# Kernel tuning notes

Measured on AMD Instinct MI355X. Metric: run time of the kernel, lower is better.

The kernel has to match this reference:

```python
import jax, jax.numpy as jnp
import numpy as np

N = 50000      # nodes
E = 800000     # edges (before self-loops)
DIN = 128      # in_channels
DH = 64        # hidden_channels
HEADS = 2
DOUT = 64      # out_channels
NEG_SLOPE = 0.2  # PyG GATConv leaky_relu slope


def setup_inputs() -> dict:
    key = jax.random.key(0)
    ks = jax.random.split(key, 10)
    node_emb = jax.random.normal(ks[0], (N, DIN), dtype=jnp.float32)
    edge_index = jax.random.randint(ks[1], (2, E), 0, N, dtype=jnp.int64)
    # conv1: in -> hidden, heads=2, concat=True
    W1 = jax.random.normal(ks[2], (DIN, HEADS * DH), dtype=jnp.float32) / np.sqrt(DIN)
    att_src1 = jax.random.normal(ks[3], (HEADS, DH), dtype=jnp.float32) * 0.1
    att_dst1 = jax.random.normal(ks[4], (HEADS, DH), dtype=jnp.float32) * 0.1
    b1 = jnp.zeros((HEADS * DH,), dtype=jnp.float32)
    # conv2: hidden*heads -> out, heads=1, concat=False
    W2 = jax.random.normal(ks[5], (HEADS * DH, 1 * DOUT), dtype=jnp.float32) / np.sqrt(HEADS * DH)
    att_src2 = jax.random.normal(ks[6], (1, DOUT), dtype=jnp.float32) * 0.1
    att_dst2 = jax.random.normal(ks[7], (1, DOUT), dtype=jnp.float32) * 0.1
    b2 = jnp.zeros((DOUT,), dtype=jnp.float32)
    return {"node_emb": node_emb, "edge_index": edge_index,
            "W1": W1, "att_src1": att_src1, "att_dst1": att_dst1, "b1": b1,
            "W2": W2, "att_src2": att_src2, "att_dst2": att_dst2, "b2": b2}


def gat_layer(x, src, dst, W, att_src, att_dst, bias, heads, concat, n):
    # x: [N, Fin]; W: [Fin, heads*C]; att_*: [heads, C]
    C = W.shape[1] // heads
    h = (x @ W).reshape(n, heads, C)                       # [N, H, C]
    a_src = jnp.einsum('nhc,hc->nh', h, att_src)           # [N, H]
    a_dst = jnp.einsum('nhc,hc->nh', h, att_dst)           # [N, H]
    e = jax.nn.leaky_relu(a_src[src] + a_dst[dst], NEG_SLOPE)  # [E, H]
    # segment softmax over incoming edges of each destination node
    m = jax.ops.segment_max(e, dst, num_segments=n)        # [N, H]
    ex = jnp.exp(e - m[dst])
    denom = jax.ops.segment_sum(ex, dst, num_segments=n)   # [N, H]
    alpha = ex / denom[dst]                                # [E, H]
    out = jax.ops.segment_sum(h[src] * alpha[:, :, None], dst, num_segments=n)  # [N, H, C]
    if concat:
        out = out.reshape(n, heads * C)
    else:
        out = out.mean(axis=1)
    return out + bias


def reference(node_emb, edge_index, W1, att_src1, att_dst1, b1, W2, att_src2, att_dst2, b2):
    loops = jnp.arange(N, dtype=edge_index.dtype)
    src = jnp.concatenate([edge_index[0], loops])  # PyG add_self_loops=True
    dst = jnp.concatenate([edge_index[1], loops])
    h = gat_layer(node_emb, src, dst, W1, att_src1, att_dst1, b1, HEADS, True, N)
    h = jax.nn.elu(h)
    # dropout is identity in eval mode
    out = gat_layer(h, src, dst, W2, att_src2, att_dst2, b2, 1, False, N)
    return out
```

## Files before the change

### kernel.cpp

```cpp
#include <hip/hip_runtime.h>
#include <hip/hip_fp16.h>
#include <math.h>

constexpr float NEG_SLOPE = 0.2f;
constexpr int NPART = 8;
constexpr int WSLOT = 16;

__device__ inline __half2 u2h(unsigned int u) { return *reinterpret_cast<__half2*>(&u); }
__device__ inline unsigned int h2u(__half2 h) { return *reinterpret_cast<unsigned int*>(&h); }

__device__ inline void fmamix8(uint4 v, float al, float* acc) {
    float2 f0 = __half22float2(u2h(v.x)), f1 = __half22float2(u2h(v.y));
    float2 f2 = __half22float2(u2h(v.z)), f3 = __half22float2(u2h(v.w));
    acc[0] = fmaf(al, f0.x, acc[0]); acc[1] = fmaf(al, f0.y, acc[1]);
    acc[2] = fmaf(al, f1.x, acc[2]); acc[3] = fmaf(al, f1.y, acc[3]);
    acc[4] = fmaf(al, f2.x, acc[4]); acc[5] = fmaf(al, f2.y, acc[5]);
    acc[6] = fmaf(al, f3.x, acc[6]); acc[7] = fmaf(al, f3.y, acc[7]);
}

__device__ inline int ell_resolve(const unsigned short* __restrict__ ell,
                                  const int* pre, int node, int n, int l) {
    int p = 0;
#pragma unroll
    for (int t = 1; t < NPART; t++)
        if (l >= pre[t]) p = t;
    int slot = l - pre[p];
    return (int)ell[((size_t)p * n + node) * WSLOT + slot];
}

__global__ __launch_bounds__(256) void k_fused1(
    const int* __restrict__ src, const int* __restrict__ dst, int e, int S, int G,
    int* __restrict__ cur, unsigned short* __restrict__ ell,
    const float* __restrict__ x, const float* __restrict__ W,
    const float* __restrict__ a_src, const float* __restrict__ a_dst,
    __half* __restrict__ h1h, float* __restrict__ att, int n) {
    __shared__ float xs[32 * 128];
    __shared__ __half wsh[128 * 128];
    int bid = blockIdx.x;
    int t = threadIdx.x;

    int third = bid / 3;
    bool interleave = (2 * S <= G + 2);
    bool isScat = interleave ? ((bid % 3 == 0) && (third < S)) : (bid < S);
    if (isScat) {
        int sid = interleave ? third : bid;
        int p = bid & (NPART - 1);
        int i0 = (sid * 256 + t) * 4;
        if (i0 + 3 < e) {
            int4 d4 = *reinterpret_cast<const int4*>(dst + i0);
            int4 s4 = *reinterpret_cast<const int4*>(src + i0);
            int a0 = atomicAdd(&cur[p * n + d4.x], 1);
            int a1 = atomicAdd(&cur[p * n + d4.y], 1);
            int a2 = atomicAdd(&cur[p * n + d4.z], 1);
            int a3 = atomicAdd(&cur[p * n + d4.w], 1);
            if (a0 < WSLOT) ell[((size_t)p * n + d4.x) * WSLOT + a0] = (unsigned short)s4.x;
            if (a1 < WSLOT) ell[((size_t)p * n + d4.y) * WSLOT + a1] = (unsigned short)s4.y;
            if (a2 < WSLOT) ell[((size_t)p * n + d4.z) * WSLOT + a2] = (unsigned short)s4.z;
            if (a3 < WSLOT) ell[((size_t)p * n + d4.w) * WSLOT + a3] = (unsigned short)s4.w;
        } else {
            for (int i = i0; i < e; i++) {
                int d = dst[i];
                int slot = atomicAdd(&cur[p * n + d], 1);
                if (slot < WSLOT) ell[((size_t)p * n + d) * WSLOT + slot] = (unsigned short)src[i];
            }
        }
        return;
    }
    int gid = interleave ? (bid - min(S, (bid + 2) / 3)) : (bid - S);
    if (gid >= G) return;

    const float4* Wv = (const float4*)W;
    uint2* wsv = (uint2*)wsh;
#pragma unroll
    for (int i = 0; i < 16; i++) {
        float4 w = Wv[t + 256 * i];
        __half2 a = __floats2half2_rn(w.x, w.y);
        __half2 b = __floats2half2_rn(w.z, w.w);
        uint2 o; o.x = h2u(a); o.y = h2u(b);
        wsv[t + 256 * i] = o;
    }
    int row0 = gid * 32;
    const float4* xv = (const float4*)x;
    float4* xsv = (float4*)xs;
#pragma unroll
    for (int ii = 0; ii < 4; ii++) {
        int i = t + 256 * ii;
        int r = i >> 5, c4 = i & 31;
        int gr = row0 + r;
        float4 v = (gr < n) ? xv[(size_t)gr * 32 + c4] : make_float4(0.f, 0.f, 0.f, 0.f);
        xsv[i] = v;
    }
    __syncthreads();
    int tc = t & 31;
    int tr = t >> 5;
    float acc[4][4];
#pragma unroll
    for (int i = 0; i < 4; i++)
#pragma unroll
        for (int j = 0; j < 4; j++) acc[i][j] = 0.f;
    const uint2* wsv2 = (const uint2*)wsh;
    for (int k = 0; k < 128; k++) {
        uint2 wu = wsv2[k * 32 + tc];
        float2 wA = __half22float2(u2h(wu.x));
        float2 wB = __half22float2(u2h(wu.y));
#pragma unroll
        for (int i = 0; i < 4; i++) {
            float xvv = xs[(tr * 4 + i) * 128 + k];
            acc[i][0] = fmaf(xvv, wA.x, acc[i][0]);
            acc[i][1] = fmaf(xvv, wA.y, acc[i][1]);
            acc[i][2] = fmaf(xvv, wB.x, acc[i][2]);
            acc[i][3] = fmaf(xvv, wB.y, acc[i][3]);
        }
    }
#pragma unroll
    for (int i = 0; i < 4; i++) {
        int gr = row0 + tr * 4 + i;
        if (gr < n) {
            __half2 p01 = __floats2half2_rn(acc[i][0], acc[i][1]);
            __half2 p23 = __floats2half2_rn(acc[i][2], acc[i][3]);
            uint2 o; o.x = h2u(p01); o.y = h2u(p23);
            *reinterpret_cast<uint2*>(h1h + (size_t)gr * 128 + 4 * tc) = o;
        }
    }
    const float4* asv = (const float4*)a_src;
    const float4* adv = (const float4*)a_dst;
    float4 as4 = asv[tc], ad4 = adv[tc];
    int lane = t & 63;
#pragma unroll
    for (int i = 0; i < 4; i++) {
        float s = acc[i][0] * as4.x + acc[i][1] * as4.y + acc[i][2] * as4.z + acc[i][3] * as4.w;
        float d = acc[i][0] * ad4.x + acc[i][1] * ad4.y + acc[i][2] * ad4.z + acc[i][3] * ad4.w;
#pragma unroll
        for (int o = 1; o < 16; o <<= 1) {
            s += __shfl_xor(s, o);
            d += __shfl_xor(d, o);
        }
        float s1 = __shfl(s, (lane & 32) + 16);
        float d1 = __shfl(d, (lane & 32) + 16);
        int gr = row0 + tr * 4 + i;
        if ((lane & 31) == 0 && gr < n) {
            ((float4*)att)[gr] = make_float4(s, s1, d, d1);
        }
    }
}

__global__ __launch_bounds__(256) void k_gemm2(const __half* __restrict__ x2h,
                                               const float* __restrict__ W,
                                               const float* __restrict__ a_src,
                                               const float* __restrict__ a_dst,
                                               __half* __restrict__ h2h,
                                               float* __restrict__ att, int n) {
    __shared__ float xs[32 * 128];
    __shared__ __half wsh[128 * 64];
    int t = threadIdx.x;
    const float4* Wv = (const float4*)W;
    uint2* wsv = (uint2*)wsh;
#pragma unroll
    for (int i = 0; i < 8; i++) {
        float4 w = Wv[t + 256 * i];
        __half2 a = __floats2half2_rn(w.x, w.y);
        __half2 b = __floats2half2_rn(w.z, w.w);
        uint2 o; o.x = h2u(a); o.y = h2u(b);
        wsv[t + 256 * i] = o;
    }
    int row0 = blockIdx.x * 32;
    const uint2* xv = (const uint2*)x2h;
    float4* xsv = (float4*)xs;
#pragma unroll
    for (int ii = 0; ii < 4; ii++) {
        int i = t + 256 * ii;
        int r = i >> 5, c4 = i & 31;
        int gr = row0 + r;
        uint2 u = (gr < n) ? xv[(size_t)gr * 32 + c4] : make_uint2(0u, 0u);
        float2 lo = __half22float2(u2h(u.x)), hi = __half22float2(u2h(u.y));
        xsv[i] = make_float4(lo.x, lo.y, hi.x, hi.y);
    }
    __syncthreads();
    int tc = t & 15;
    int tr = t >> 4;
    float acc[2][4];
#pragma unroll
    for (int i = 0; i < 2; i++)
#pragma unroll
        for (int j = 0; j < 4; j++) acc[i][j] = 0.f;
    const uint2* wsv2 = (const uint2*)wsh;
    for (int k = 0; k < 128; k++) {
        uint2 wu = wsv2[k * 16 + tc];
        float2 wA = __half22float2(u2h(wu.x));
        float2 wB = __half22float2(u2h(wu.y));
#pragma unroll
        for (int i = 0; i < 2; i++) {
            float xvv = xs[(tr * 2 + i) * 128 + k];
            acc[i][0] = fmaf(xvv, wA.x, acc[i][0]);
            acc[i][1] = fmaf(xvv, wA.y, acc[i][1]);
            acc[i][2] = fmaf(xvv, wB.x, acc[i][2]);
            acc[i][3] = fmaf(xvv, wB.y, acc[i][3]);
        }
    }
#pragma unroll
    for (int i = 0; i < 2; i++) {
        int gr = row0 + tr * 2 + i;
        if (gr < n) {
            __half2 p01 = __floats2half2_rn(acc[i][0], acc[i][1]);
            __half2 p23 = __floats2half2_rn(acc[i][2], acc[i][3]);
            uint2 o; o.x = h2u(p01); o.y = h2u(p23);
            *reinterpret_cast<uint2*>(h2h + (size_t)gr * 64 + 4 * tc) = o;
        }
    }
    const float4* asv = (const float4*)a_src;
    const float4* adv = (const float4*)a_dst;
    float4 as4 = asv[tc], ad4 = adv[tc];
#pragma unroll
    for (int i = 0; i < 2; i++) {
        float s = acc[i][0] * as4.x + acc[i][1] * as4.y + acc[i][2] * as4.z + acc[i][3] * as4.w;
        float d = acc[i][0] * ad4.x + acc[i][1] * ad4.y + acc[i][2] * ad4.z + acc[i][3] * ad4.w;
#pragma unroll
        for (int o = 1; o < 16; o <<= 1) {
            s += __shfl_xor(s, o);
            d += __shfl_xor(d, o);
        }
        int gr = row0 + tr * 2 + i;
        if (tc == 0 && gr < n) {
            ((float2*)att)[gr] = make_float2(s, d);
        }
    }
}

__global__ __launch_bounds__(256) void k_aggr1(const int* __restrict__ cur,
                                               const unsigned short* __restrict__ ell,
                                               const float* __restrict__ att,
                                               const __half* __restrict__ h1h,
                                               const float* __restrict__ bias,
                                               __half* __restrict__ x2h, int n) {
    int wid = threadIdx.x >> 6, lane = threadIdx.x & 63;
    int node = blockIdx.x * 4 + wid;
    if (node >= n) return;

    int cnt = 0;
    if (lane < NPART) cnt = cur[lane * n + node];
    int pre[NPART];
    int tot = 1;
#pragma unroll
    for (int p = 0; p < NPART; p++) {
        int cc = __shfl(cnt, p);
        cc = cc < WSLOT ? cc : WSLOT;
        pre[p] = tot;
        tot += cc;
    }

    const float4* attv = (const float4*)att;
    float4 an = attv[node];
    float ad0 = an.z, ad1 = an.w;

    int chq = lane & 15;
    int g = lane >> 4;
    bool hsel = (chq >= 8);

    float f[8];

    if (tot <= 64) {
        int c = node;
        float p0 = 0.f, p1 = 0.f;
        if (lane < tot) {
            if (lane > 0) c = ell_resolve(ell, pre, node, n, lane);
            float4 a = attv[c];
            float e0 = a.x + ad0; e0 = e0 > 0.f ? e0 : NEG_SLOPE * e0;
            float e1 = a.y + ad1; e1 = e1 > 0.f ? e1 : NEG_SLOPE * e1;
            p0 = __expf(e0); p1 = __expf(e1);
        }
        float sum0 = p0, sum1 = p1;
#pragma unroll
        for (int d = 1; d < 64; d <<= 1) {
            sum0 += __shfl_xor(sum0, d);
            sum1 += __shfl_xor(sum1, d);
        }
        float rsel = hsel ? (1.f / sum1) : (1.f / sum0);

        __half2 z = __float2half2_rn(0.f);
        __half2 hacc0 = z, hacc1 = z, hacc2 = z, hacc3 = z;
        for (int k0 = 0; k0 < tot; k0 += 16) {
            uint4 v[4];
            __half2 al2[4];
#pragma unroll
            for (int u = 0; u < 4; u++) {
                int k = k0 + 4 * u + g;
                int ks = k & 63;
                int sn = __shfl(c, ks);
                float pa = __shfl(p0, ks);
                float pb = __shfl(p1, ks);
                float alf = (k < tot) ? (hsel ? pb : pa) * rsel : 0.f;
                al2[u] = __float2half2_rn(alf);
                v[u] = *reinterpret_cast<const uint4*>(h1h + (size_t)sn * 128 + 8 * chq);
            }
#pragma unroll
            for (int u = 0; u < 4; u++) {
                hacc0 = __hfma2(al2[u], u2h(v[u].x), hacc0);
                hacc1 = __hfma2(al2[u], u2h(v[u].y), hacc1);
                hacc2 = __hfma2(al2[u], u2h(v[u].z), hacc2);
                hacc3 = __hfma2(al2[u], u2h(v[u].w), hacc3);
            }
        }
        f[0] = __low2float(hacc0); f[1] = __high2float(hacc0);
        f[2] = __low2float(hacc1); f[3] = __high2float(hacc1);
        f[4] = __low2float(hacc2); f[5] = __high2float(hacc2);
        f[6] = __low2float(hacc3); f[7] = __high2float(hacc3);
    } else {
        float sum0 = 0.f, sum1 = 0.f;
        for (int l = lane; l < tot; l += 64) {
            int c = (l == 0) ? node : ell_resolve(ell, pre, node, n, l);
            float4 a = attv[c];
            float e0 = a.x + ad0; e0 = e0 > 0.f ? e0 : NEG_SLOPE * e0;
            float e1 = a.y + ad1; e1 = e1 > 0.f ? e1 : NEG_SLOPE * e1;
            sum0 += __expf(e0); sum1 += __expf(e1);
        }
#pragma unroll
        for (int d = 1; d < 64; d <<= 1) {
            sum0 += __shfl_xor(sum0, d);
            sum1 += __shfl_xor(sum1, d);
        }
        float rsel = hsel ? (1.f / sum1) : (1.f / sum0);
        float acc[8];
#pragma unroll
        for (int i = 0; i < 8; i++) acc[i] = 0.f;
        for (int j = 0; j < tot; j += 4) {
            int l = j + g;
            bool valid = (l < tot);
            int lc = valid ? l : 0;
            int sn = (lc == 0) ? node : ell_resolve(ell, pre, node, n, lc);
            float4 a = attv[sn];
            float e0 = a.x + ad0; e0 = e0 > 0.f ? e0 : NEG_SLOPE * e0;
            float e1 = a.y + ad1; e1 = e1 > 0.f ? e1 : NEG_SLOPE * e1;
            float pp = hsel ? __expf(e1) : __expf(e0);
            float al = valid ? pp * rsel : 0.f;
            uint4 v = *reinterpret_cast<const uint4*>(h1h + (size_t)sn * 128 + 8 * chq);
            fmamix8(v, al, acc);
        }
#pragma unroll
        for (int i = 0; i < 8; i++) f[i] = acc[i];
    }

#pragma unroll
    for (int i = 0; i < 8; i++) {
        f[i] += __shfl_xor(f[i], 16);
        f[i] += __shfl_xor(f[i], 32);
    }
    if (lane < 16) {
        const float4* bv = (const float4*)bias;
        float4 bA = bv[2 * chq], bB = bv[2 * chq + 1];
        float o[8];
        o[0] = f[0] + bA.x; o[1] = f[1] + bA.y;
        o[2] = f[2] + bA.z; o[3] = f[3] + bA.w;
        o[4] = f[4] + bB.x; o[5] = f[5] + bB.y;
        o[6] = f[6] + bB.z; o[7] = f[7] + bB.w;
#pragma unroll
        for (int i = 0; i < 8; i++) o[i] = o[i] > 0.f ? o[i] : (__expf(o[i]) - 1.f);
        __half2 q01 = __floats2half2_rn(o[0], o[1]);
        __half2 q23 = __floats2half2_rn(o[2], o[3]);
        __half2 q45 = __floats2half2_rn(o[4], o[5]);
        __half2 q67 = __floats2half2_rn(o[6], o[7]);
        uint4 w; w.x = h2u(q01); w.y = h2u(q23); w.z = h2u(q45); w.w = h2u(q67);
        *reinterpret_cast<uint4*>(x2h + (size_t)node * 128 + 8 * chq) = w;
    }
}

__global__ __launch_bounds__(256) void k_aggr2(const int* __restrict__ cur,
                                               const unsigned short* __restrict__ ell,
                                               const float* __restrict__ att,
                                               const __half* __restrict__ h2h,
                                               const float* __restrict__ bias,
                                               float* __restrict__ out, int n) {
    int wid = threadIdx.x >> 6, lane = threadIdx.x & 63;
    int node = blockIdx.x * 4 + wid;
    if (node >= n) return;

    int cnt = 0;
    if (lane < NPART) cnt = cur[lane * n + node];
    int pre[NPART];
    int tot = 1;
#pragma unroll
    for (int p = 0; p < NPART; p++) {
        int cc = __shfl(cnt, p);
        cc = cc < WSLOT ? cc : WSLOT;
        pre[p] = tot;
        tot += cc;
    }

    const float2* attv = (const float2*)att;
    float adn = attv[node].y;
    int chq = lane & 7;
    int g = lane >> 3;

    float f[8];

    if (tot <= 64) {
        int c = node;
        float p = 0.f;
        if (lane < tot) {
            if (lane > 0) c = ell_resolve(ell, pre, node, n, lane);
            float e = attv[c].x + adn;
            e = e > 0.f ? e : NEG_SLOPE * e;
            p = __expf(e);
        }
        float sum = p;
#pragma unroll
        for (int d = 1; d < 64; d <<= 1) sum += __shfl_xor(sum, d);
        float r = 1.f / sum;

        __half2 z = __float2half2_rn(0.f);
        __half2 hacc0 = z, hacc1 = z, hacc2 = z, hacc3 = z;
        for (int k0 = 0; k0 < tot; k0 += 16) {
            uint4 v[2];
            __half2 al2[2];
#pragma unroll
            for (int u = 0; u < 2; u++) {
                int k = k0 + 8 * u + g;
                int ks = k & 63;
                int sn = __shfl(c, ks);
                float pk = __shfl(p, ks);
                float alf = (k < tot) ? pk * r : 0.f;
                al2[u] = __float2half2_rn(alf);
                v[u] = *reinterpret_cast<const uint4*>(h2h + (size_t)sn * 64 + 8 * chq);
            }
#pragma unroll
            for (int u = 0; u < 2; u++) {
                hacc0 = __hfma2(al2[u], u2h(v[u].x), hacc0);
                hacc1 = __hfma2(al2[u], u2h(v[u].y), hacc1);
                hacc2 = __hfma2(al2[u], u2h(v[u].z), hacc2);
                hacc3 = __hfma2(al2[u], u2h(v[u].w), hacc3);
            }
        }
        f[0] = __low2float(hacc0); f[1] = __high2float(hacc0);
        f[2] = __low2float(hacc1); f[3] = __high2float(hacc1);
        f[4] = __low2float(hacc2); f[5] = __high2float(hacc2);
        f[6] = __low2float(hacc3); f[7] = __high2float(hacc3);
    } else {
        float sum = 0.f;
        for (int l = lane; l < tot; l += 64) {
            int c = (l == 0) ? node : ell_resolve(ell, pre, node, n, l);
            float e = attv[c].x + adn;
            e = e > 0.f ? e : NEG_SLOPE * e;
            sum += __expf(e);
        }
#pragma unroll
        for (int d = 1; d < 64; d <<= 1) sum += __shfl_xor(sum, d);
        float r = 1.f / sum;
        float acc[8];
#pragma unroll
        for (int i = 0; i < 8; i++) acc[i] = 0.f;
        for (int j = 0; j < tot; j += 8) {
            int l = j + g;
            bool valid = (l < tot);
            int lc = valid ? l : 0;
            int sn = (lc == 0) ? node : ell_resolve(ell, pre, node, n, lc);
            float e = attv[sn].x + adn;
            e = e > 0.f ? e : NEG_SLOPE * e;
            float al = valid ? __expf(e) * r : 0.f;
            uint4 v = *reinterpret_cast<const uint4*>(h2h + (size_t)sn * 64 + 8 * chq);
            fmamix8(v, al, acc);
        }
#pragma unroll
        for (int i = 0; i < 8; i++) f[i] = acc[i];
    }

#pragma unroll
    for (int i = 0; i < 8; i++) {
        f[i] += __shfl_xor(f[i], 8);
        f[i] += __shfl_xor(f[i], 16);
        f[i] += __shfl_xor(f[i], 32);
    }
    if (lane < 8) {
        const float4* bv = (const float4*)bias;
        float4 bA = bv[2 * chq], bB = bv[2 * chq + 1];
        float4* ov = (float4*)(out + (size_t)node * 64 + 8 * chq);
        ov[0] = make_float4(f[0] + bA.x, f[1] + bA.y, f[2] + bA.z, f[3] + bA.w);
        ov[1] = make_float4(f[4] + bB.x, f[5] + bB.y, f[6] + bB.z, f[7] + bB.w);
    }
}

extern "C" void kernel_launch(void* const* d_in, const int* in_sizes, int n_in,
                              void* d_out, int out_size, void* d_ws, size_t ws_size,
                              hipStream_t stream) {
    const float* x    = (const float*)d_in[0];
    const int*   ei   = (const int*)d_in[1];
    const float* W1   = (const float*)d_in[2];
    const float* asr1 = (const float*)d_in[3];
    const float* adt1 = (const float*)d_in[4];
    const float* b1   = (const float*)d_in[5];
    const float* W2   = (const float*)d_in[6];
    const float* asr2 = (const float*)d_in[7];
    const float* adt2 = (const float*)d_in[8];
    const float* b2   = (const float*)d_in[9];
    float* out = (float*)d_out;

    const int N = in_sizes[0] / 128;
    const int E = in_sizes[1] / 2;
    const int* srcI = ei;
    const int* dstI = ei + E;

    char* p = (char*)d_ws;
    auto alloc = [&](size_t b) -> void* {
        void* r = (void*)p;
        p += ((b + 255) / 256) * 256;
        return r;
    };
    int* cur = (int*)alloc(sizeof(int) * (size_t)NPART * N);
    unsigned short* ell = (unsigned short*)alloc(sizeof(unsigned short) *
                                                 (size_t)NPART * N * WSLOT);
    __half* h1h = (__half*)alloc(sizeof(__half) * (size_t)N * 128);
    float* att1 = (float*)alloc(sizeof(float) * (size_t)N * 4);
    __half* x2h = (__half*)alloc(sizeof(__half) * (size_t)N * 128);
    __half* h2h = (__half*)alloc(sizeof(__half) * (size_t)N * 64);
    float* att2 = (float*)alloc(sizeof(float) * (size_t)N * 2);

    int S = (E + 1023) / 1024;
    int G = (N + 31) / 32;
    int nbNode4 = (N + 3) / 4;
    int nbRow32 = (N + 31) / 32;

    hipMemsetAsync(cur, 0, sizeof(int) * (size_t)NPART * N, stream);

    k_fused1<<<S + G, 256, 0, stream>>>(srcI, dstI, E, S, G, cur, ell,
                                        x, W1, asr1, adt1, h1h, att1, N);

    k_aggr1<<<nbNode4, 256, 0, stream>>>(cur, ell, att1, h1h, b1, x2h, N);

    k_gemm2<<<nbRow32, 256, 0, stream>>>(x2h, W2, asr2, adt2, h2h, att2, N);
    k_aggr2<<<nbNode4, 256, 0, stream>>>(cur, ell, att2, h2h, b2, out, N);
}
```

Measured before the change: 146.3 us.

## Use fp16 dot2 GEMMs with pre-transposed weights and XCC-based scatter partitions

Adds a small kernel that converts W1/W2 to fp16 transposed layout once per call. Both GEMMs then keep fp16 x and W tiles in shared memory and use the fdot2 instruction on 8-element vectors, which removes per-block weight conversion and halves shared-memory traffic. The column mapping changes to strided columns, so h1h/h2h are now written as scalar half stores. The edge scatter picks its partition from the hardware XCC id instead of the block id, keeping atomics local to one die's L2. The risks are fp16 products feeding fp32 accumulation, an extra launch, and less coalesced output stores.

```diff
diff --git a/kernel.cpp b/kernel.cpp
--- a/kernel.cpp
+++ b/kernel.cpp
@@ -6,8 +6,30 @@
 constexpr int NPART = 8;
 constexpr int WSLOT = 16;
 
+typedef _Float16 __attribute__((ext_vector_type(2))) h2v;
+
 __device__ inline __half2 u2h(unsigned int u) { return *reinterpret_cast<__half2*>(&u); }
 __device__ inline unsigned int h2u(__half2 h) { return *reinterpret_cast<unsigned int*>(&h); }
+
+__device__ inline float dot8(uint4 a, uint4 b, float c) {
+#if __has_builtin(__builtin_amdgcn_fdot2)
+    c = __builtin_amdgcn_fdot2(__builtin_bit_cast(h2v, a.x), __builtin_bit_cast(h2v, b.x), c, false);
+    c = __builtin_amdgcn_fdot2(__builtin_bit_cast(h2v, a.y), __builtin_bit_cast(h2v, b.y), c, false);
+    c = __builtin_amdgcn_fdot2(__builtin_bit_cast(h2v, a.z), __builtin_bit_cast(h2v, b.z), c, false);
+    c = __builtin_amdgcn_fdot2(__builtin_bit_cast(h2v, a.w), __builtin_bit_cast(h2v, b.w), c, false);
+#else
+    float2 fa, fb;
+    fa = __half22float2(u2h(a.x)); fb = __half22float2(u2h(b.x));
+    c = fmaf(fa.x, fb.x, c); c = fmaf(fa.y, fb.y, c);
+    fa = __half22float2(u2h(a.y)); fb = __half22float2(u2h(b.y));
+    c = fmaf(fa.x, fb.x, c); c = fmaf(fa.y, fb.y, c);
+    fa = __half22float2(u2h(a.z)); fb = __half22float2(u2h(b.z));
+    c = fmaf(fa.x, fb.x, c); c = fmaf(fa.y, fb.y, c);
+    fa = __half22float2(u2h(a.w)); fb = __half22float2(u2h(b.w));
+    c = fmaf(fa.x, fb.x, c); c = fmaf(fa.y, fb.y, c);
+#endif
+    return c;
+}
 
 __device__ inline void fmamix8(uint4 v, float al, float* acc) {
     float2 f0 = __half22float2(u2h(v.x)), f1 = __half22float2(u2h(v.y));
@@ -28,14 +50,29 @@
     return (int)ell[((size_t)p * n + node) * WSLOT + slot];
 }
 
+__global__ void k_wt(const float* __restrict__ W1, const float* __restrict__ W2,
+                     __half* __restrict__ Wt1, __half* __restrict__ Wt2) {
+    int id = blockIdx.x * 256 + threadIdx.x;
+    if (id < 128 * 128) {
+        int col = id >> 7, k = id & 127;
+        Wt1[id] = __float2half(W1[k * 128 + col]);
+    } else {
+        int j = id - 128 * 128;
+        if (j < 64 * 128) {
+            int col = j >> 7, k = j & 127;
+            Wt2[j] = __float2half(W2[k * 64 + col]);
+        }
+    }
+}
+
 __global__ __launch_bounds__(256) void k_fused1(
     const int* __restrict__ src, const int* __restrict__ dst, int e, int S, int G,
     int* __restrict__ cur, unsigned short* __restrict__ ell,
-    const float* __restrict__ x, const float* __restrict__ W,
+    const float* __restrict__ x, const __half* __restrict__ Wt1,
     const float* __restrict__ a_src, const float* __restrict__ a_dst,
     __half* __restrict__ h1h, float* __restrict__ att, int n) {
-    __shared__ float xs[32 * 128];
-    __shared__ __half wsh[128 * 128];
+    __shared__ __half xsh[32 * 128];
+    __shared__ __half wsh[128 * 72];
     int bid = blockIdx.x;
     int t = threadIdx.x;
 
@@ -44,7 +81,9 @@
     bool isScat = interleave ? ((bid % 3 == 0) && (third < S)) : (bid < S);
     if (isScat) {
         int sid = interleave ? third : bid;
-        int p = bid & (NPART - 1);
+        unsigned xcc;
+        asm volatile("s_getreg_b32 %0, hwreg(HW_REG_XCC_ID)" : "=s"(xcc));
+        int p = (int)(xcc & (NPART - 1));
         int i0 = (sid * 256 + t) * 4;
         if (i0 + 3 < e) {
             int4 d4 = *reinterpret_cast<const int4*>(dst + i0);
@@ -69,157 +108,156 @@
     int gid = interleave ? (bid - min(S, (bid + 2) / 3)) : (bid - S);
     if (gid >= G) return;
 
-    const float4* Wv = (const float4*)W;
-    uint2* wsv = (uint2*)wsh;
-#pragma unroll
-    for (int i = 0; i < 16; i++) {
-        float4 w = Wv[t + 256 * i];
-        __half2 a = __floats2half2_rn(w.x, w.y);
-        __half2 b = __floats2half2_rn(w.z, w.w);
-        uint2 o; o.x = h2u(a); o.y = h2u(b);
-        wsv[t + 256 * i] = o;
-    }
     int row0 = gid * 32;
+    int tc = t & 31;
+    int tr = t >> 5;
+
     const float4* xv = (const float4*)x;
-    float4* xsv = (float4*)xs;
 #pragma unroll
     for (int ii = 0; ii < 4; ii++) {
         int i = t + 256 * ii;
         int r = i >> 5, c4 = i & 31;
         int gr = row0 + r;
         float4 v = (gr < n) ? xv[(size_t)gr * 32 + c4] : make_float4(0.f, 0.f, 0.f, 0.f);
-        xsv[i] = v;
-    }
-    __syncthreads();
-    int tc = t & 31;
-    int tr = t >> 5;
+        __half2 a = __floats2half2_rn(v.x, v.y);
+        __half2 b = __floats2half2_rn(v.z, v.w);
+        uint2 o; o.x = h2u(a); o.y = h2u(b);
+        *reinterpret_cast<uint2*>(xsh + r * 128 + c4 * 4) = o;
+    }
+
     float acc[4][4];
 #pragma unroll
     for (int i = 0; i < 4; i++)
 #pragma unroll
         for (int j = 0; j < 4; j++) acc[i][j] = 0.f;
-    const uint2* wsv2 = (const uint2*)wsh;
-    for (int k = 0; k < 128; k++) {
-        uint2 wu = wsv2[k * 32 + tc];
-        float2 wA = __half22float2(u2h(wu.x));
-        float2 wB = __half22float2(u2h(wu.y));
-#pragma unroll
-        for (int i = 0; i < 4; i++) {
-            float xvv = xs[(tr * 4 + i) * 128 + k];
-            acc[i][0] = fmaf(xvv, wA.x, acc[i][0]);
-            acc[i][1] = fmaf(xvv, wA.y, acc[i][1]);
-            acc[i][2] = fmaf(xvv, wB.x, acc[i][2]);
-            acc[i][3] = fmaf(xvv, wB.y, acc[i][3]);
-        }
-    }
+
+#pragma unroll
+    for (int kh = 0; kh < 2; kh++) {
+        __syncthreads();
+#pragma unroll
+        for (int ii = 0; ii < 4; ii++) {
+            int i = t + 256 * ii;
+            int col = i >> 3, kg = i & 7;
+            uint4 w = *reinterpret_cast<const uint4*>(Wt1 + col * 128 + kh * 64 + kg * 8);
+            *reinterpret_cast<uint4*>(wsh + col * 72 + kg * 8) = w;
+        }
+        __syncthreads();
+#pragma unroll
+        for (int k8 = 0; k8 < 8; k8++) {
+            int kbase = kh * 64 + k8 * 8;
+            uint4 ax[4], wx[4];
+#pragma unroll
+            for (int i = 0; i < 4; i++)
+                ax[i] = *reinterpret_cast<const uint4*>(xsh + (4 * tr + i) * 128 + kbase);
+#pragma unroll
+            for (int j = 0; j < 4; j++)
+                wx[j] = *reinterpret_cast<const uint4*>(wsh + (tc + 32 * j) * 72 + k8 * 8);
+#pragma unroll
+            for (int i = 0; i < 4; i++)
+#pragma unroll
+                for (int j = 0; j < 4; j++)
+                    acc[i][j] = dot8(ax[i], wx[j], acc[i][j]);
+        }
+    }
+
+    float as0 = a_src[tc], as1 = a_src[tc + 32], as2 = a_src[tc + 64], as3 = a_src[tc + 96];
+    float ad0 = a_dst[tc], ad1 = a_dst[tc + 32], ad2 = a_dst[tc + 64], ad3 = a_dst[tc + 96];
 #pragma unroll
     for (int i = 0; i < 4; i++) {
-        int gr = row0 + tr * 4 + i;
+        int gr = row0 + 4 * tr + i;
         if (gr < n) {
-            __half2 p01 = __floats2half2_rn(acc[i][0], acc[i][1]);
-            __half2 p23 = __floats2half2_rn(acc[i][2], acc[i][3]);
-            uint2 o; o.x = h2u(p01); o.y = h2u(p23);
-            *reinterpret_cast<uint2*>(h1h + (size_t)gr * 128 + 4 * tc) = o;
-        }
-    }
-    const float4* asv = (const float4*)a_src;
-    const float4* adv = (const float4*)a_dst;
-    float4 as4 = asv[tc], ad4 = adv[tc];
-    int lane = t & 63;
-#pragma unroll
-    for (int i = 0; i < 4; i++) {
-        float s = acc[i][0] * as4.x + acc[i][1] * as4.y + acc[i][2] * as4.z + acc[i][3] * as4.w;
-        float d = acc[i][0] * ad4.x + acc[i][1] * ad4.y + acc[i][2] * ad4.z + acc[i][3] * ad4.w;
-#pragma unroll
-        for (int o = 1; o < 16; o <<= 1) {
-            s += __shfl_xor(s, o);
-            d += __shfl_xor(d, o);
-        }
-        float s1 = __shfl(s, (lane & 32) + 16);
-        float d1 = __shfl(d, (lane & 32) + 16);
-        int gr = row0 + tr * 4 + i;
-        if ((lane & 31) == 0 && gr < n) {
-            ((float4*)att)[gr] = make_float4(s, s1, d, d1);
+#pragma unroll
+            for (int j = 0; j < 4; j++)
+                h1h[(size_t)gr * 128 + tc + 32 * j] = __float2half(acc[i][j]);
+        }
+        float s0 = acc[i][0] * as0 + acc[i][1] * as1;
+        float s1 = acc[i][2] * as2 + acc[i][3] * as3;
+        float d0 = acc[i][0] * ad0 + acc[i][1] * ad1;
+        float d1 = acc[i][2] * ad2 + acc[i][3] * ad3;
+#pragma unroll
+        for (int o = 1; o < 32; o <<= 1) {
+            s0 += __shfl_xor(s0, o);
+            s1 += __shfl_xor(s1, o);
+            d0 += __shfl_xor(d0, o);
+            d1 += __shfl_xor(d1, o);
+        }
+        if (tc == 0 && gr < n) {
+            ((float4*)att)[gr] = make_float4(s0, s1, d0, d1);
         }
     }
 }
 
 __global__ __launch_bounds__(256) void k_gemm2(const __half* __restrict__ x2h,
-                                               const float* __restrict__ W,
+                                               const __half* __restrict__ Wt2,
                                                const float* __restrict__ a_src,
                                                const float* __restrict__ a_dst,
                                                __half* __restrict__ h2h,
                                                float* __restrict__ att, int n) {
-    __shared__ float xs[32 * 128];
-    __shared__ __half wsh[128 * 64];
+    __shared__ __half xsh[32 * 128];
+    __shared__ __half wsh[64 * 136];
     int t = threadIdx.x;
-    const float4* Wv = (const float4*)W;
-    uint2* wsv = (uint2*)wsh;
-#pragma unroll
-    for (int i = 0; i < 8; i++) {
-        float4 w = Wv[t + 256 * i];
-        __half2 a = __floats2half2_rn(w.x, w.y);
-        __half2 b = __floats2half2_rn(w.z, w.w);
-        uint2 o; o.x = h2u(a); o.y = h2u(b);
-        wsv[t + 256 * i] = o;
-    }
     int row0 = blockIdx.x * 32;
-    const uint2* xv = (const uint2*)x2h;
-    float4* xsv = (float4*)xs;
+    int tc = t & 15;
+    int tr = t >> 4;
+
+#pragma unroll
+    for (int ii = 0; ii < 2; ii++) {
+        int i = t + 256 * ii;
+        int r = i >> 4, g8 = i & 15;
+        int gr = row0 + r;
+        uint4 v = (gr < n) ? *reinterpret_cast<const uint4*>(x2h + (size_t)gr * 128 + g8 * 8)
+                           : make_uint4(0u, 0u, 0u, 0u);
+        *reinterpret_cast<uint4*>(xsh + r * 128 + g8 * 8) = v;
+    }
 #pragma unroll
     for (int ii = 0; ii < 4; ii++) {
         int i = t + 256 * ii;
-        int r = i >> 5, c4 = i & 31;
-        int gr = row0 + r;
-        uint2 u = (gr < n) ? xv[(size_t)gr * 32 + c4] : make_uint2(0u, 0u);
-        float2 lo = __half22float2(u2h(u.x)), hi = __half22float2(u2h(u.y));
-        xsv[i] = make_float4(lo.x, lo.y, hi.x, hi.y);
+        int col = i >> 4, kg = i & 15;
+        uint4 w = *reinterpret_cast<const uint4*>(Wt2 + col * 128 + kg * 8);
+        *reinterpret_cast<uint4*>(wsh + col * 136 + kg * 8) = w;
     }
     __syncthreads();
-    int tc = t & 15;
-    int tr = t >> 4;
+
     float acc[2][4];
 #pragma unroll
     for (int i = 0; i < 2; i++)
 #pragma unroll
         for (int j = 0; j < 4; j++) acc[i][j] = 0.f;
-    const uint2* wsv2 = (const uint2*)wsh;
-    for (int k = 0; k < 128; k++) {
-        uint2 wu = wsv2[k * 16 + tc];
-        float2 wA = __half22float2(u2h(wu.x));
-        float2 wB = __half22float2(u2h(wu.y));
-#pragma unroll
-        for (int i = 0; i < 2; i++) {
-            float xvv = xs[(tr * 2 + i) * 128 + k];
-            acc[i][0] = fmaf(xvv, wA.x, acc[i][0]);
-            acc[i][1] = fmaf(xvv, wA.y, acc[i][1]);
-            acc[i][2] = fmaf(xvv, wB.x, acc[i][2]);
-            acc[i][3] = fmaf(xvv, wB.y, acc[i][3]);
-        }
-    }
+
+#pragma unroll
+    for (int k8 = 0; k8 < 16; k8++) {
+        uint4 ax[2], wx[4];
+#pragma unroll
+        for (int i = 0; i < 2; i++)
+            ax[i] = *reinterpret_cast<const uint4*>(xsh + (2 * tr + i) * 128 + k8 * 8);
+#pragma unroll
+        for (int j = 0; j < 4; j++)
+            wx[j] = *reinterpret_cast<const uint4*>(wsh + (tc + 16 * j) * 136 + k8 * 8);
+#pragma unroll
+        for (int i = 0; i < 2; i++)
+#pragma unroll
+            for (int j = 0; j < 4; j++)
+                acc[i][j] = dot8(ax[i], wx[j], acc[i][j]);
+    }
+
+    float as[4], ad[4];
+#pragma unroll
+    for (int j = 0; j < 4; j++) { as[j] = a_src[tc + 16 * j]; ad[j] = a_dst[tc + 16 * j]; }
 #pragma unroll
     for (int i = 0; i < 2; i++) {
-        int gr = row0 + tr * 2 + i;
+        int gr = row0 + 2 * tr + i;
         if (gr < n) {
-            __half2 p01 = __floats2half2_rn(acc[i][0], acc[i][1]);
-            __half2 p23 = __floats2half2_rn(acc[i][2], acc[i][3]);
-            uint2 o; o.x = h2u(p01); o.y = h2u(p23);
-            *reinterpret_cast<uint2*>(h2h + (size_t)gr * 64 + 4 * tc) = o;
-        }
-    }
-    const float4* asv = (const float4*)a_src;
-    const float4* adv = (const float4*)a_dst;
-    float4 as4 = asv[tc], ad4 = adv[tc];
-#pragma unroll
-    for (int i = 0; i < 2; i++) {
-        float s = acc[i][0] * as4.x + acc[i][1] * as4.y + acc[i][2] * as4.z + acc[i][3] * as4.w;
-        float d = acc[i][0] * ad4.x + acc[i][1] * ad4.y + acc[i][2] * ad4.z + acc[i][3] * ad4.w;
+#pragma unroll
+            for (int j = 0; j < 4; j++)
+                h2h[(size_t)gr * 64 + tc + 16 * j] = __float2half(acc[i][j]);
+        }
+        float s = acc[i][0] * as[0] + acc[i][1] * as[1] + acc[i][2] * as[2] + acc[i][3] * as[3];
+        float d = acc[i][0] * ad[0] + acc[i][1] * ad[1] + acc[i][2] * ad[2] + acc[i][3] * ad[3];
 #pragma unroll
         for (int o = 1; o < 16; o <<= 1) {
             s += __shfl_xor(s, o);
             d += __shfl_xor(d, o);
         }
-        int gr = row0 + tr * 2 + i;
         if (tc == 0 && gr < n) {
             ((float2*)att)[gr] = make_float2(s, d);
         }
@@ -511,6 +549,8 @@
     __half* x2h = (__half*)alloc(sizeof(__half) * (size_t)N * 128);
     __half* h2h = (__half*)alloc(sizeof(__half) * (size_t)N * 64);
     float* att2 = (float*)alloc(sizeof(float) * (size_t)N * 2);
+    __half* Wt1 = (__half*)alloc(sizeof(__half) * 128 * 128);
+    __half* Wt2 = (__half*)alloc(sizeof(__half) * 64 * 128);
 
     int S = (E + 1023) / 1024;
     int G = (N + 31) / 32;
@@ -519,11 +559,13 @@
 
     hipMemsetAsync(cur, 0, sizeof(int) * (size_t)NPART * N, stream);
 
+    k_wt<<<96, 256, 0, stream>>>(W1, W2, Wt1, Wt2);
+
     k_fused1<<<S + G, 256, 0, stream>>>(srcI, dstI, E, S, G, cur, ell,
-                                        x, W1, asr1, adt1, h1h, att1, N);
+                                        x, Wt1, asr1, adt1, h1h, att1, N);
 
     k_aggr1<<<nbNode4, 256, 0, stream>>>(cur, ell, att1, h1h, b1, x2h, N);
 
-    k_gemm2<<<nbRow32, 256, 0, stream>>>(x2h, W2, asr2, adt2, h2h, att2, N);
+    k_gemm2<<<nbRow32, 256, 0, stream>>>(x2h, Wt2, asr2, adt2, h2h, att2, N);
     k_aggr2<<<nbNode4, 256, 0, stream>>>(cur, ell, att2, h2h, b2, out, N);
 }
```

Result: slower. 161.0 us (+10.1%).

## Interleave ELL partitions per node and stage W in two halves

Applied to the files above, without the earlier changes.

Changes the per-partition count and ELL neighbor arrays from partition-major to node-major. All partitions of a destination node now sit next to each other, so the aggregation kernels read counts and neighbor slots from one contiguous region instead of eight strided ones. Separately, the GEMM block now converts and stages the weight matrix in two 64-row halves with extra barriers, halving its shared memory to raise occupancy. The cost is an extra sync round and a reload of shared memory per half. Scatter atomics from different partitions may now contend on nearby cache lines.

```diff
diff --git a/kernel.cpp b/kernel.cpp
--- a/kernel.cpp
+++ b/kernel.cpp
@@ -19,13 +19,13 @@
 }
 
 __device__ inline int ell_resolve(const unsigned short* __restrict__ ell,
-                                  const int* pre, int node, int n, int l) {
+                                  const int* pre, int node, int l) {
     int p = 0;
 #pragma unroll
     for (int t = 1; t < NPART; t++)
         if (l >= pre[t]) p = t;
     int slot = l - pre[p];
-    return (int)ell[((size_t)p * n + node) * WSLOT + slot];
+    return (int)ell[((size_t)node * NPART + p) * WSLOT + slot];
 }
 
 __global__ __launch_bounds__(256) void k_fused1(
@@ -35,7 +35,7 @@
     const float* __restrict__ a_src, const float* __restrict__ a_dst,
     __half* __restrict__ h1h, float* __restrict__ att, int n) {
     __shared__ float xs[32 * 128];
-    __shared__ __half wsh[128 * 128];
+    __shared__ __half wsh[64 * 128];
     int bid = blockIdx.x;
     int t = threadIdx.x;
 
@@ -49,19 +49,19 @@
         if (i0 + 3 < e) {
             int4 d4 = *reinterpret_cast<const int4*>(dst + i0);
             int4 s4 = *reinterpret_cast<const int4*>(src + i0);
-            int a0 = atomicAdd(&cur[p * n + d4.x], 1);
-            int a1 = atomicAdd(&cur[p * n + d4.y], 1);
-            int a2 = atomicAdd(&cur[p * n + d4.z], 1);
-            int a3 = atomicAdd(&cur[p * n + d4.w], 1);
-            if (a0 < WSLOT) ell[((size_t)p * n + d4.x) * WSLOT + a0] = (unsigned short)s4.x;
-            if (a1 < WSLOT) ell[((size_t)p * n + d4.y) * WSLOT + a1] = (unsigned short)s4.y;
-            if (a2 < WSLOT) ell[((size_t)p * n + d4.z) * WSLOT + a2] = (unsigned short)s4.z;
-            if (a3 < WSLOT) ell[((size_t)p * n + d4.w) * WSLOT + a3] = (unsigned short)s4.w;
+            int a0 = atomicAdd(&cur[d4.x * NPART + p], 1);
+            int a1 = atomicAdd(&cur[d4.y * NPART + p], 1);
+            int a2 = atomicAdd(&cur[d4.z * NPART + p], 1);
+            int a3 = atomicAdd(&cur[d4.w * NPART + p], 1);
+            if (a0 < WSLOT) ell[((size_t)d4.x * NPART + p) * WSLOT + a0] = (unsigned short)s4.x;
+            if (a1 < WSLOT) ell[((size_t)d4.y * NPART + p) * WSLOT + a1] = (unsigned short)s4.y;
+            if (a2 < WSLOT) ell[((size_t)d4.z * NPART + p) * WSLOT + a2] = (unsigned short)s4.z;
+            if (a3 < WSLOT) ell[((size_t)d4.w * NPART + p) * WSLOT + a3] = (unsigned short)s4.w;
         } else {
             for (int i = i0; i < e; i++) {
                 int d = dst[i];
-                int slot = atomicAdd(&cur[p * n + d], 1);
-                if (slot < WSLOT) ell[((size_t)p * n + d) * WSLOT + slot] = (unsigned short)src[i];
+                int slot = atomicAdd(&cur[d * NPART + p], 1);
+                if (slot < WSLOT) ell[((size_t)d * NPART + p) * WSLOT + slot] = (unsigned short)src[i];
             }
         }
         return;
@@ -69,16 +69,6 @@
     int gid = interleave ? (bid - min(S, (bid + 2) / 3)) : (bid - S);
     if (gid >= G) return;
 
-    const float4* Wv = (const float4*)W;
-    uint2* wsv = (uint2*)wsh;
-#pragma unroll
-    for (int i = 0; i < 16; i++) {
-        float4 w = Wv[t + 256 * i];
-        __half2 a = __floats2half2_rn(w.x, w.y);
-        __half2 b = __floats2half2_rn(w.z, w.w);
-        uint2 o; o.x = h2u(a); o.y = h2u(b);
-        wsv[t + 256 * i] = o;
-    }
     int row0 = gid * 32;
     const float4* xv = (const float4*)x;
     float4* xsv = (float4*)xs;
@@ -90,7 +80,7 @@
         float4 v = (gr < n) ? xv[(size_t)gr * 32 + c4] : make_float4(0.f, 0.f, 0.f, 0.f);
         xsv[i] = v;
     }
-    __syncthreads();
+
     int tc = t & 31;
     int tr = t >> 5;
     float acc[4][4];
@@ -98,20 +88,38 @@
     for (int i = 0; i < 4; i++)
 #pragma unroll
         for (int j = 0; j < 4; j++) acc[i][j] = 0.f;
+
+    const float4* Wv = (const float4*)W;
+    uint2* wsv = (uint2*)wsh;
     const uint2* wsv2 = (const uint2*)wsh;
-    for (int k = 0; k < 128; k++) {
-        uint2 wu = wsv2[k * 32 + tc];
-        float2 wA = __half22float2(u2h(wu.x));
-        float2 wB = __half22float2(u2h(wu.y));
-#pragma unroll
-        for (int i = 0; i < 4; i++) {
-            float xvv = xs[(tr * 4 + i) * 128 + k];
-            acc[i][0] = fmaf(xvv, wA.x, acc[i][0]);
-            acc[i][1] = fmaf(xvv, wA.y, acc[i][1]);
-            acc[i][2] = fmaf(xvv, wB.x, acc[i][2]);
-            acc[i][3] = fmaf(xvv, wB.y, acc[i][3]);
-        }
-    }
+#pragma unroll
+    for (int kh = 0; kh < 2; kh++) {
+        __syncthreads();
+#pragma unroll
+        for (int ii = 0; ii < 8; ii++) {
+            int i = t + 256 * ii;
+            float4 w = Wv[kh * 2048 + i];
+            __half2 a = __floats2half2_rn(w.x, w.y);
+            __half2 b = __floats2half2_rn(w.z, w.w);
+            uint2 o; o.x = h2u(a); o.y = h2u(b);
+            wsv[i] = o;
+        }
+        __syncthreads();
+        for (int kk = 0; kk < 64; kk++) {
+            uint2 wu = wsv2[kk * 32 + tc];
+            float2 wA = __half22float2(u2h(wu.x));
+            float2 wB = __half22float2(u2h(wu.y));
+#pragma unroll
+            for (int i = 0; i < 4; i++) {
+                float xvv = xs[(tr * 4 + i) * 128 + kh * 64 + kk];
+                acc[i][0] = fmaf(xvv, wA.x, acc[i][0]);
+                acc[i][1] = fmaf(xvv, wA.y, acc[i][1]);
+                acc[i][2] = fmaf(xvv, wB.x, acc[i][2]);
+                acc[i][3] = fmaf(xvv, wB.y, acc[i][3]);
+            }
+        }
+    }
+
 #pragma unroll
     for (int i = 0; i < 4; i++) {
         int gr = row0 + tr * 4 + i;
@@ -237,7 +245,7 @@
     if (node >= n) return;
 
     int cnt = 0;
-    if (lane < NPART) cnt = cur[lane * n + node];
+    if (lane < NPART) cnt = cur[node * NPART + lane];
     int pre[NPART];
     int tot = 1;
 #pragma unroll
@@ -262,7 +270,7 @@
         int c = node;
         float p0 = 0.f, p1 = 0.f;
         if (lane < tot) {
-            if (lane > 0) c = ell_resolve(ell, pre, node, n, lane);
+            if (lane > 0) c = ell_resolve(ell, pre, node, lane);
             float4 a = attv[c];
             float e0 = a.x + ad0; e0 = e0 > 0.f ? e0 : NEG_SLOPE * e0;
             float e1 = a.y + ad1; e1 = e1 > 0.f ? e1 : NEG_SLOPE * e1;
@@ -307,7 +315,7 @@
     } else {
         float sum0 = 0.f, sum1 = 0.f;
         for (int l = lane; l < tot; l += 64) {
-            int c = (l == 0) ? node : ell_resolve(ell, pre, node, n, l);
+            int c = (l == 0) ? node : ell_resolve(ell, pre, node, l);
             float4 a = attv[c];
             float e0 = a.x + ad0; e0 = e0 > 0.f ? e0 : NEG_SLOPE * e0;
             float e1 = a.y + ad1; e1 = e1 > 0.f ? e1 : NEG_SLOPE * e1;
@@ -326,7 +334,7 @@
             int l = j + g;
             bool valid = (l < tot);
             int lc = valid ? l : 0;
-            int sn = (lc == 0) ? node : ell_resolve(ell, pre, node, n, lc);
+            int sn = (lc == 0) ? node : ell_resolve(ell, pre, node, lc);
             float4 a = attv[sn];
             float e0 = a.x + ad0; e0 = e0 > 0.f ? e0 : NEG_SLOPE * e0;
             float e1 = a.y + ad1; e1 = e1 > 0.f ? e1 : NEG_SLOPE * e1;
@@ -374,7 +382,7 @@
     if (node >= n) return;
 
     int cnt = 0;
-    if (lane < NPART) cnt = cur[lane * n + node];
+    if (lane < NPART) cnt = cur[node * NPART + lane];
     int pre[NPART];
     int tot = 1;
 #pragma unroll
@@ -396,7 +404,7 @@
         int c = node;
         float p = 0.f;
         if (lane < tot) {
-            if (lane > 0) c = ell_resolve(ell, pre, node, n, lane);
+            if (lane > 0) c = ell_resolve(ell, pre, node, lane);
             float e = attv[c].x + adn;
             e = e > 0.f ? e : NEG_SLOPE * e;
             p = __expf(e);
@@ -436,7 +444,7 @@
     } else {
         float sum = 0.f;
         for (int l = lane; l < tot; l += 64) {
-            int c = (l == 0) ? node : ell_resolve(ell, pre, node, n, l);
+            int c = (l == 0) ? node : ell_resolve(ell, pre, node, l);
             float e = attv[c].x + adn;
             e = e > 0.f ? e : NEG_SLOPE * e;
             sum += __expf(e);
@@ -451,7 +459,7 @@
             int l = j + g;
             bool valid = (l < tot);
             int lc = valid ? l : 0;
-            int sn = (lc == 0) ? node : ell_resolve(ell, pre, node, n, lc);
+            int sn = (lc == 0) ? node : ell_resolve(ell, pre, node, lc);
             float e = attv[sn].x + adn;
             e = e > 0.f ? e : NEG_SLOPE * e;
             float al = valid ? __expf(e) * r : 0.f;
```

New measurement: 144.7 us. No clear change (-1.1%).
